# Kernel tuning notes

Hardware: AMD Instinct MI355X
Metric: run time of the kernel (lower is better)

Reference implementation:

```python
import jax, jax.numpy as jnp
import numpy as np


def setup_inputs() -> dict:
    key = jax.random.key(0)
    k1, k2, k3 = jax.random.split(key, 3)
    B, C, H, W = 16, 256, 48, 48
    INTER = C // 2
    x = jax.random.normal(k1, (B, C, H, W), dtype=jnp.float32)
    # nn.init.normal_(weight, std=0.01); 1x1 conv kernels stored as (out, in)
    theta_w = 0.01 * jax.random.normal(k2, (INTER, C), dtype=jnp.float32)
    phi_w = 0.01 * jax.random.normal(k3, (INTER, C), dtype=jnp.float32)
    theta_b = jnp.zeros((INTER,), dtype=jnp.float32)
    phi_b = jnp.zeros((INTER,), dtype=jnp.float32)
    return {"x": x, "theta_w": theta_w, "theta_b": theta_b, "phi_w": phi_w, "phi_b": phi_b}


def reference(x, theta_w, theta_b, phi_w, phi_b):
    b, c, h, w = x.shape
    inter = theta_w.shape[0]
    n = h * w
    # 1x1 conv == channel-wise linear projection
    theta_x = jnp.einsum('bchw,kc->bkhw', x, theta_w) + theta_b[None, :, None, None]
    phi_x = jnp.einsum('bchw,kc->bkhw', x, phi_w) + phi_b[None, :, None, None]
    q = theta_x.reshape(b, inter, n)   # [b, k, n]
    kmat = phi_x.reshape(b, inter, n)  # [b, k, n]
    g = x.reshape(b, c, n)             # [b, c, n]
    # f = theta^T @ phi : [b, n, n], scaled then softmaxed over last dim
    f = jnp.einsum('bkn,bkm->bnm', q, kmat) / jnp.sqrt(jnp.asarray(inter, x.dtype))
    f = jax.nn.softmax(f, axis=-1)
    # y = f @ g^T : [b, c, n]
    y = jnp.einsum('bnm,bcm->bcn', f, g)
    return y.reshape(b, c, h, w)
```

## Files before the change

### kernel.cpp

```cpp
#include <hip/hip_runtime.h>
#include <hip/hip_bf16.h>

#define B_SZ 16
#define C_IN 256
#define N_SP 2304
#define K_INT 128
#define NTILE 36
#define MT 32
#define MITER 72

typedef __attribute__((ext_vector_type(8))) short short8;
typedef __attribute__((ext_vector_type(4))) float f32x4;

__device__ __align__(16) short g_Wbf[2 * K_INT * C_IN];

__device__ inline unsigned pk_bf16(float a, float b) {
  float2 f; f.x = a; f.y = b;
  __hip_bfloat162 h = __float22bfloat162_rn(f);
  unsigned u;
  __builtin_memcpy(&u, &h, sizeof(u));
  return u;
}

__global__ __launch_bounds__(256) void wcvt_kernel(
    const float* __restrict__ tw, const float* __restrict__ pw)
{
  const int i = (blockIdx.x * 256 + threadIdx.x) * 4;
  float4 a = *(const float4*)(tw + i);
  float4 p = *(const float4*)(pw + i);
  uint2 ua; ua.x = pk_bf16(a.x, a.y); ua.y = pk_bf16(a.z, a.w);
  uint2 up; up.x = pk_bf16(p.x, p.y); up.y = pk_bf16(p.z, p.w);
  *(uint2*)(g_Wbf + i) = ua;
  *(uint2*)(g_Wbf + 32768 + i) = up;
}

__global__ __launch_bounds__(256) void proj_kernel(
    const float* __restrict__ x,
    const float* __restrict__ theta_b, const float* __restrict__ phi_b,
    short* __restrict__ Qt, short* __restrict__ Kt, short* __restrict__ Gbf)
{
  __shared__ short Xl[64][264];

  const int b  = blockIdx.x / NTILE;
  const int n0 = (blockIdx.x % NTILE) * 64;
  const int t  = threadIdx.x;

  {
    const int cr = t >> 4;
    const int a  = t & 15;
    const int n  = a * 4;
    const int g8 = (a & 3) << 3;
    const float* xs = x + ((size_t)b * C_IN + cr) * N_SP + n0 + n;
    short* gs = Gbf + ((size_t)b * C_IN + cr) * N_SP + n0 + n;
#pragma unroll
    for (int i = 0; i < 16; ++i) {
      float4 v = *(const float4*)(xs + (size_t)i * 16 * N_SP);
      unsigned p0 = pk_bf16(v.x, v.y), p1 = pk_bf16(v.z, v.w);
      uint2 u; u.x = p0; u.y = p1;
      *(uint2*)(gs + (size_t)i * 16 * N_SP) = u;
      const int cs0 = (cr + 16 * i) ^ g8;
      Xl[n + 0][cs0] = (short)p0;
      Xl[n + 1][cs0] = (short)(p0 >> 16);
      Xl[n + 2][cs0] = (short)p1;
      Xl[n + 3][cs0] = (short)(p1 >> 16);
    }
  }
  __syncthreads();

  const int wave = t >> 6, lane = t & 63;
  const int col = lane & 15, quad = lane >> 4;
  const int rg8 = ((col >> 2) & 3) << 3;

  f32x4 acc[2][2][4];
#pragma unroll
  for (int p = 0; p < 2; ++p)
#pragma unroll
    for (int kr = 0; kr < 2; ++kr)
#pragma unroll
      for (int j = 0; j < 4; ++j) {
        acc[p][kr][j][0] = 0.f; acc[p][kr][j][1] = 0.f;
        acc[p][kr][j][2] = 0.f; acc[p][kr][j][3] = 0.f;
      }

#pragma unroll
  for (int cs = 0; cs < 8; ++cs) {
    const int c0 = cs * 32;
    short8 afr[2][2];
#pragma unroll
    for (int p = 0; p < 2; ++p)
#pragma unroll
      for (int kr = 0; kr < 2; ++kr) {
        const int k = wave * 32 + kr * 16 + col;
        afr[p][kr] = *(const short8*)(g_Wbf + p * 32768 + k * C_IN + c0 + quad * 8);
      }
#pragma unroll
    for (int j = 0; j < 4; ++j) {
      short8 bfr = *(const short8*)&Xl[j * 16 + col][(c0 + quad * 8) ^ rg8];
#pragma unroll
      for (int p = 0; p < 2; ++p)
#pragma unroll
        for (int kr = 0; kr < 2; ++kr)
          acc[p][kr][j] = __builtin_amdgcn_mfma_f32_16x16x32_bf16(
              afr[p][kr], bfr, acc[p][kr][j], 0, 0, 0);
    }
  }

#pragma unroll
  for (int p = 0; p < 2; ++p) {
    const float* bias = p ? phi_b : theta_b;
    short* dst = p ? Kt : Qt;
#pragma unroll
    for (int kr = 0; kr < 2; ++kr) {
      const int k0 = wave * 32 + kr * 16 + quad * 4;
      float4 bv = *(const float4*)(bias + k0);
#pragma unroll
      for (int j = 0; j < 4; ++j) {
        const int n = n0 + j * 16 + col;
        f32x4 v = acc[p][kr][j];
        uint2 sv;
        sv.x = pk_bf16(v[0] + bv.x, v[1] + bv.y);
        sv.y = pk_bf16(v[2] + bv.z, v[3] + bv.w);
        *(uint2*)(dst + ((size_t)b * N_SP + n) * K_INT + k0) = sv;
      }
    }
  }
}

__global__ __launch_bounds__(256) void attn_kernel(
    const short* __restrict__ Qt, const short* __restrict__ Kt,
    const short* __restrict__ Gbf, float* __restrict__ out)
{
  __shared__ __align__(16) char Kl[2][8192];
  __shared__ __align__(16) short Pblob[2][4][64][8];
  __shared__ float l_lds[64];

  const int wg  = (blockIdx.x & 7) * 72 + (blockIdx.x >> 3);
  const int b   = wg / NTILE;
  const int qn0 = (wg % NTILE) * 64;
  const int t = threadIdx.x;
  const int wave = t >> 6, lane = t & 63;
  const int col = lane & 15, quad = lane >> 4;

  const short* Ktb = Kt  + (size_t)b * N_SP * K_INT;
  const short* Gb  = Gbf + (size_t)b * C_IN * N_SP;

  short8 qf[4];
  {
    const short* qb = Qt + ((size_t)b * N_SP + qn0 + wave * 16 + col) * K_INT + quad * 8;
#pragma unroll
    for (int kk = 0; kk < 4; ++kk) qf[kk] = *(const short8*)(qb + kk * 32);
  }

  f32x4 yacc[4][4];
#pragma unroll
  for (int i = 0; i < 4; ++i)
#pragma unroll
    for (int j = 0; j < 4; ++j) {
      yacc[i][j][0] = 0.f; yacc[i][j][1] = 0.f;
      yacc[i][j][2] = 0.f; yacc[i][j][3] = 0.f;
    }
  f32x4 lacc;
  lacc[0] = 0.f; lacc[1] = 0.f; lacc[2] = 0.f; lacc[3] = 0.f;

  short8 ones;
#pragma unroll
  for (int j = 0; j < 8; ++j) ones[j] = (short)0x3F80;

  const float SC2 = 0.12754859f;

  const int KW = (t >> 4) * 256 + ((((t & 15) ^ ((t >> 4) & 7))) << 4);
  int KR0[4];
#pragma unroll
  for (int kk = 0; kk < 4; ++kk)
    KR0[kk] = col * 256 + ((((kk << 2) + quad) ^ (col & 7)) << 4);

  const int koff = (t >> 4) * K_INT + (t & 15) * 8;
  const short* gbase = Gb + ((size_t)(wave * 64 + col)) * N_SP + quad * 8;

  short8 krA, krB;
  krA = *(const short8*)(Ktb + koff);
  krB = *(const short8*)(Ktb + 2048 + koff);
  *(short8*)(Kl[0] + KW) = krA;
  *(short8*)(Kl[0] + KW + 4096) = krB;
  krA = *(const short8*)(Ktb + 4096 + koff);
  krB = *(const short8*)(Ktb + 6144 + koff);
  short8 gA[4], gB[4];
#pragma unroll
  for (int ct = 0; ct < 4; ++ct)
    gA[ct] = *(const short8*)(gbase + (size_t)ct * 16 * N_SP);
  __syncthreads();

#define SUBITER(MTV, CUR, GC, GN)                                              \
  {                                                                            \
                           \
    f32x4 s0, s1;                                                              \
    s0[0] = 0.f; s0[1] = 0.f; s0[2] = 0.f; s0[3] = 0.f;                        \
    s1[0] = 0.f; s1[1] = 0.f; s1[2] = 0.f; s1[3] = 0.f;                        \
    _Pragma("unroll")                                                          \
    for (int kk = 0; kk < 4; ++kk) {                                           \
      short8 a0 = *(const short8*)(Kl[CUR] + KR0[kk]);                         \
      s0 = __builtin_amdgcn_mfma_f32_16x16x32_bf16(a0, qf[kk], s0, 0, 0, 0);   \
      short8 a1 = *(const short8*)(Kl[CUR] + KR0[kk] + 4096);                  \
      s1 = __builtin_amdgcn_mfma_f32_16x16x32_bf16(a1, qf[kk], s1, 0, 0, 0);   \
    }                                                                          \
                    \
    unsigned u0 = pk_bf16(exp2f(s0[0] * SC2), exp2f(s0[1] * SC2));             \
    unsigned u1 = pk_bf16(exp2f(s0[2] * SC2), exp2f(s0[3] * SC2));             \
    unsigned u2 = pk_bf16(exp2f(s1[0] * SC2), exp2f(s1[1] * SC2));             \
    unsigned u3 = pk_bf16(exp2f(s1[2] * SC2), exp2f(s1[3] * SC2));             \
    asm("v_permlane32_swap_b32 %0, %1" : "+v"(u0), "+v"(u2));                  \
    asm("v_permlane32_swap_b32 %0, %1" : "+v"(u1), "+v"(u3));                  \
    asm("v_permlane16_swap_b32 %0, %1" : "+v"(u0), "+v"(u2));                  \
    asm("v_permlane16_swap_b32 %0, %1" : "+v"(u1), "+v"(u3));                  \
    unsigned uu[4] = {u0, u1, u2, u3};                                         \
    short8 pa; __builtin_memcpy(&pa, uu, 16);                                  \
    lacc = __builtin_amdgcn_mfma_f32_16x16x32_bf16(pa, ones, lacc, 0, 0, 0);   \
                         \
    *(short8*)&Pblob[CUR][wave][lane][0] = pa;                                 \
        \
    if ((MTV) + 1 < MITER) {                                                   \
      *(short8*)(Kl[(CUR) ^ 1] + KW) = krA;                                    \
      *(short8*)(Kl[(CUR) ^ 1] + KW + 4096) = krB;                             \
    }                                                                          \
    __syncthreads();                                                           \
        \
    if ((MTV) + 2 < MITER) {                                                   \
      const short* kp = Ktb + (size_t)((MTV) + 2) * 4096 + koff;               \
      krA = *(const short8*)(kp);                                              \
      krB = *(const short8*)(kp + 2048);                                       \
    }                                                                          \
          \
    if ((MTV) + 1 < MITER) {                                                   \
      _Pragma("unroll")                                                        \
      for (int ct = 0; ct < 4; ++ct)                                           \
        GN[ct] = *(const short8*)(gbase + (size_t)ct * 16 * N_SP +             \
                                  ((MTV) + 1) * 32);                           \
    }                                                                          \
             \
    _Pragma("unroll")                                                          \
    for (int qt = 0; qt < 4; ++qt) {                                           \
      short8 paq = *(const short8*)&Pblob[CUR][qt][lane][0];                   \
      _Pragma("unroll")                                                        \
      for (int ct = 0; ct < 4; ++ct)                                           \
        yacc[qt][ct] = __builtin_amdgcn_mfma_f32_16x16x32_bf16(                \
            paq, GC[ct], yacc[qt][ct], 0, 0, 0);                               \
    }                                                                          \
  }

  for (int mt2 = 0; mt2 < MITER / 2; ++mt2) {
    SUBITER(2 * mt2,     0, gA, gB)
    SUBITER(2 * mt2 + 1, 1, gB, gA)
  }
#undef SUBITER

  if (col == 0) {
#pragma unroll
    for (int r = 0; r < 4; ++r) l_lds[wave * 16 + quad * 4 + r] = lacc[r];
  }
  __syncthreads();

#pragma unroll
  for (int qt = 0; qt < 4; ++qt) {
    float4 lq = *(const float4*)&l_lds[qt * 16 + quad * 4];
    float4 iv;
    iv.x = 1.0f / lq.x; iv.y = 1.0f / lq.y; iv.z = 1.0f / lq.z; iv.w = 1.0f / lq.w;
    const int nb = qn0 + qt * 16 + quad * 4;
#pragma unroll
    for (int ct = 0; ct < 4; ++ct) {
      const int c = wave * 64 + ct * 16 + col;
      f32x4 v = yacc[qt][ct];
      float4 o;
      o.x = v[0] * iv.x; o.y = v[1] * iv.y; o.z = v[2] * iv.z; o.w = v[3] * iv.w;
      *(float4*)(out + ((size_t)b * C_IN + c) * N_SP + nb) = o;
    }
  }
}

extern "C" void kernel_launch(void* const* d_in, const int* in_sizes, int n_in,
                              void* d_out, int out_size, void* d_ws, size_t ws_size,
                              hipStream_t stream) {
  const float* x  = (const float*)d_in[0];
  const float* tw = (const float*)d_in[1];
  const float* tb = (const float*)d_in[2];
  const float* pw = (const float*)d_in[3];
  const float* pb = (const float*)d_in[4];
  float* out = (float*)d_out;

  short* Qt  = (short*)d_ws;
  short* Kt  = Qt + (size_t)B_SZ * N_SP * K_INT;
  short* Gbf = Kt + (size_t)B_SZ * N_SP * K_INT;

  wcvt_kernel<<<32, 256, 0, stream>>>(tw, pw);
  proj_kernel<<<B_SZ * NTILE, 256, 0, stream>>>(x, tb, pb, Qt, Kt, Gbf);
  attn_kernel<<<B_SZ * NTILE, 256, 0, stream>>>(Qt, Kt, Gbf, out);
}
```

Measured before the change: 263.7 us.

## Double key tile per pipeline step to halve barriers in attention loop

Doubles the key-tile width processed per iteration from 32 to 64 positions, so each step computes four score MFMAs per k-slice, two P fragments, and sixteen extra PV MFMAs. It halves the number of __syncthreads barriers and prefetch rounds over the key dimension, and moves the global prefetches for K and G before the barrier. It also drops the block-index swizzle across XCDs. In exchange it uses more registers (8 G fragments, 4 K prefetch regs) and twice the LDS, which may lower occupancy, and the removed swizzle may hurt L2 locality.

```diff
diff --git a/kernel.cpp b/kernel.cpp
--- a/kernel.cpp
+++ b/kernel.cpp
@@ -6,8 +6,8 @@
 #define N_SP 2304
 #define K_INT 128
 #define NTILE 36
-#define MT 32
-#define MITER 72
+#define MT 64
+#define EITER 36
 
 typedef __attribute__((ext_vector_type(8))) short short8;
 typedef __attribute__((ext_vector_type(4))) float f32x4;
@@ -130,13 +130,12 @@
     const short* __restrict__ Qt, const short* __restrict__ Kt,
     const short* __restrict__ Gbf, float* __restrict__ out)
 {
-  __shared__ __align__(16) char Kl[2][8192];
-  __shared__ __align__(16) short Pblob[2][4][64][8];
+  __shared__ __align__(16) char Kl[2][16384];
+  __shared__ __align__(16) short Pblob[2][4][2][64][8];
   __shared__ float l_lds[64];
 
-  const int wg  = (blockIdx.x & 7) * 72 + (blockIdx.x >> 3);
-  const int b   = wg / NTILE;
-  const int qn0 = (wg % NTILE) * 64;
+  const int b   = blockIdx.x / NTILE;
+  const int qn0 = (blockIdx.x % NTILE) * 64;
   const int t = threadIdx.x;
   const int wave = t >> 6, lane = t & 63;
   const int col = lane & 15, quad = lane >> 4;
@@ -174,84 +173,108 @@
   for (int kk = 0; kk < 4; ++kk)
     KR0[kk] = col * 256 + ((((kk << 2) + quad) ^ (col & 7)) << 4);
 
-  const int koff = (t >> 4) * K_INT + (t & 15) * 8;
+  const int KG = (t >> 4) * K_INT + (t & 15) * 8;
   const short* gbase = Gb + ((size_t)(wave * 64 + col)) * N_SP + quad * 8;
 
-  short8 krA, krB;
-  krA = *(const short8*)(Ktb + koff);
-  krB = *(const short8*)(Ktb + 2048 + koff);
-  *(short8*)(Kl[0] + KW) = krA;
-  *(short8*)(Kl[0] + KW + 4096) = krB;
-  krA = *(const short8*)(Ktb + 4096 + koff);
-  krB = *(const short8*)(Ktb + 6144 + koff);
-  short8 gA[4], gB[4];
-#pragma unroll
-  for (int ct = 0; ct < 4; ++ct)
-    gA[ct] = *(const short8*)(gbase + (size_t)ct * 16 * N_SP);
+  short8 kr[4];
+#pragma unroll
+  for (int i = 0; i < 4; ++i) kr[i] = *(const short8*)(Ktb + KG + i * 2048);
+#pragma unroll
+  for (int i = 0; i < 4; ++i) *(short8*)(Kl[0] + KW + i * 4096) = kr[i];
+#pragma unroll
+  for (int i = 0; i < 4; ++i) kr[i] = *(const short8*)(Ktb + 8192 + KG + i * 2048);
+  short8 gA[8], gB[8];
+#pragma unroll
+  for (int i = 0; i < 8; ++i)
+    gA[i] = *(const short8*)(gbase + (size_t)(i & 3) * 16 * N_SP + (i >> 2) * 32);
   __syncthreads();
 
-#define SUBITER(MTV, CUR, GC, GN)                                              \
+#define EPOCH(EV, CUR, GC, GN)                                                 \
   {                                                                            \
-                           \
-    f32x4 s0, s1;                                                              \
-    s0[0] = 0.f; s0[1] = 0.f; s0[2] = 0.f; s0[3] = 0.f;                        \
-    s1[0] = 0.f; s1[1] = 0.f; s1[2] = 0.f; s1[3] = 0.f;                        \
+                         \
+    f32x4 s[4];                                                                \
+    _Pragma("unroll")                                                          \
+    for (int h = 0; h < 4; ++h) {                                              \
+      s[h][0] = 0.f; s[h][1] = 0.f; s[h][2] = 0.f; s[h][3] = 0.f;              \
+    }                                                                          \
     _Pragma("unroll")                                                          \
     for (int kk = 0; kk < 4; ++kk) {                                           \
-      short8 a0 = *(const short8*)(Kl[CUR] + KR0[kk]);                         \
-      s0 = __builtin_amdgcn_mfma_f32_16x16x32_bf16(a0, qf[kk], s0, 0, 0, 0);   \
-      short8 a1 = *(const short8*)(Kl[CUR] + KR0[kk] + 4096);                  \
-      s1 = __builtin_amdgcn_mfma_f32_16x16x32_bf16(a1, qf[kk], s1, 0, 0, 0);   \
-    }                                                                          \
-                    \
-    unsigned u0 = pk_bf16(exp2f(s0[0] * SC2), exp2f(s0[1] * SC2));             \
-    unsigned u1 = pk_bf16(exp2f(s0[2] * SC2), exp2f(s0[3] * SC2));             \
-    unsigned u2 = pk_bf16(exp2f(s1[0] * SC2), exp2f(s1[1] * SC2));             \
-    unsigned u3 = pk_bf16(exp2f(s1[2] * SC2), exp2f(s1[3] * SC2));             \
-    asm("v_permlane32_swap_b32 %0, %1" : "+v"(u0), "+v"(u2));                  \
-    asm("v_permlane32_swap_b32 %0, %1" : "+v"(u1), "+v"(u3));                  \
-    asm("v_permlane16_swap_b32 %0, %1" : "+v"(u0), "+v"(u2));                  \
-    asm("v_permlane16_swap_b32 %0, %1" : "+v"(u1), "+v"(u3));                  \
-    unsigned uu[4] = {u0, u1, u2, u3};                                         \
-    short8 pa; __builtin_memcpy(&pa, uu, 16);                                  \
-    lacc = __builtin_amdgcn_mfma_f32_16x16x32_bf16(pa, ones, lacc, 0, 0, 0);   \
-                         \
-    *(short8*)&Pblob[CUR][wave][lane][0] = pa;                                 \
-        \
-    if ((MTV) + 1 < MITER) {                                                   \
-      *(short8*)(Kl[(CUR) ^ 1] + KW) = krA;                                    \
-      *(short8*)(Kl[(CUR) ^ 1] + KW + 4096) = krB;                             \
+      _Pragma("unroll")                                                        \
+      for (int h = 0; h < 4; ++h) {                                            \
+        short8 a0 = *(const short8*)(Kl[CUR] + KR0[kk] + h * 4096);            \
+        s[h] = __builtin_amdgcn_mfma_f32_16x16x32_bf16(a0, qf[kk], s[h],       \
+                                                       0, 0, 0);               \
+      }                                                                        \
+    }                                                                          \
+                 \
+    short8 pa0, pa1;                                                           \
+    {                                                                          \
+      unsigned u0 = pk_bf16(exp2f(s[0][0] * SC2), exp2f(s[0][1] * SC2));       \
+      unsigned u1 = pk_bf16(exp2f(s[0][2] * SC2), exp2f(s[0][3] * SC2));       \
+      unsigned u2 = pk_bf16(exp2f(s[1][0] * SC2), exp2f(s[1][1] * SC2));       \
+      unsigned u3 = pk_bf16(exp2f(s[1][2] * SC2), exp2f(s[1][3] * SC2));       \
+      asm("v_permlane32_swap_b32 %0, %1" : "+v"(u0), "+v"(u2));                \
+      asm("v_permlane32_swap_b32 %0, %1" : "+v"(u1), "+v"(u3));                \
+      asm("v_permlane16_swap_b32 %0, %1" : "+v"(u0), "+v"(u2));                \
+      asm("v_permlane16_swap_b32 %0, %1" : "+v"(u1), "+v"(u3));                \
+      unsigned uu[4] = {u0, u1, u2, u3};                                       \
+      __builtin_memcpy(&pa0, uu, 16);                                          \
+      unsigned v0 = pk_bf16(exp2f(s[2][0] * SC2), exp2f(s[2][1] * SC2));       \
+      unsigned v1 = pk_bf16(exp2f(s[2][2] * SC2), exp2f(s[2][3] * SC2));       \
+      unsigned v2 = pk_bf16(exp2f(s[3][0] * SC2), exp2f(s[3][1] * SC2));       \
+      unsigned v3 = pk_bf16(exp2f(s[3][2] * SC2), exp2f(s[3][3] * SC2));       \
+      asm("v_permlane32_swap_b32 %0, %1" : "+v"(v0), "+v"(v2));                \
+      asm("v_permlane32_swap_b32 %0, %1" : "+v"(v1), "+v"(v3));                \
+      asm("v_permlane16_swap_b32 %0, %1" : "+v"(v0), "+v"(v2));                \
+      asm("v_permlane16_swap_b32 %0, %1" : "+v"(v1), "+v"(v3));                \
+      unsigned vv[4] = {v0, v1, v2, v3};                                       \
+      __builtin_memcpy(&pa1, vv, 16);                                          \
+    }                                                                          \
+    lacc = __builtin_amdgcn_mfma_f32_16x16x32_bf16(pa0, ones, lacc, 0, 0, 0);  \
+    lacc = __builtin_amdgcn_mfma_f32_16x16x32_bf16(pa1, ones, lacc, 0, 0, 0);  \
+                        \
+    *(short8*)&Pblob[CUR][wave][0][lane][0] = pa0;                             \
+    *(short8*)&Pblob[CUR][wave][1][lane][0] = pa1;                             \
+       \
+    if ((EV) + 1 < EITER) {                                                    \
+      _Pragma("unroll")                                                        \
+      for (int i = 0; i < 4; ++i)                                              \
+        *(short8*)(Kl[(CUR) ^ 1] + KW + i * 4096) = kr[i];                     \
+    }                                                                          \
+                     \
+    if ((EV) + 2 < EITER) {                                                    \
+      const short* kp = Ktb + (size_t)((EV) + 2) * 8192 + KG;                  \
+      _Pragma("unroll")                                                        \
+      for (int i = 0; i < 4; ++i) kr[i] = *(const short8*)(kp + i * 2048);     \
+    }                                                                          \
+              \
+    if ((EV) + 1 < EITER) {                                                    \
+      _Pragma("unroll")                                                        \
+      for (int i = 0; i < 8; ++i)                                              \
+        GN[i] = *(const short8*)(gbase + (size_t)(i & 3) * 16 * N_SP +         \
+                                 ((EV) + 1) * 64 + (i >> 2) * 32);             \
     }                                                                          \
     __syncthreads();                                                           \
-        \
-    if ((MTV) + 2 < MITER) {                                                   \
-      const short* kp = Ktb + (size_t)((MTV) + 2) * 4096 + koff;               \
-      krA = *(const short8*)(kp);                                              \
-      krB = *(const short8*)(kp + 2048);                                       \
-    }                                                                          \
-          \
-    if ((MTV) + 1 < MITER) {                                                   \
-      _Pragma("unroll")                                                        \
-      for (int ct = 0; ct < 4; ++ct)                                           \
-        GN[ct] = *(const short8*)(gbase + (size_t)ct * 16 * N_SP +             \
-                                  ((MTV) + 1) * 32);                           \
-    }                                                                          \
-             \
+              \
     _Pragma("unroll")                                                          \
     for (int qt = 0; qt < 4; ++qt) {                                           \
-      short8 paq = *(const short8*)&Pblob[CUR][qt][lane][0];                   \
-      _Pragma("unroll")                                                        \
-      for (int ct = 0; ct < 4; ++ct)                                           \
+      short8 paq0 = *(const short8*)&Pblob[CUR][qt][0][lane][0];               \
+      short8 paq1 = *(const short8*)&Pblob[CUR][qt][1][lane][0];               \
+      _Pragma("unroll")                                                        \
+      for (int ct = 0; ct < 4; ++ct) {                                         \
         yacc[qt][ct] = __builtin_amdgcn_mfma_f32_16x16x32_bf16(                \
-            paq, GC[ct], yacc[qt][ct], 0, 0, 0);                               \
-    }                                                                          \
-  }
-
-  for (int mt2 = 0; mt2 < MITER / 2; ++mt2) {
-    SUBITER(2 * mt2,     0, gA, gB)
-    SUBITER(2 * mt2 + 1, 1, gB, gA)
-  }
-#undef SUBITER
+            paq0, GC[ct], yacc[qt][ct], 0, 0, 0);                              \
+        yacc[qt][ct] = __builtin_amdgcn_mfma_f32_16x16x32_bf16(                \
+            paq1, GC[4 + ct], yacc[qt][ct], 0, 0, 0);                          \
+      }                                                                        \
+    }                                                                          \
+  }
+
+  for (int e2 = 0; e2 < EITER / 2; ++e2) {
+    EPOCH(2 * e2,     0, gA, gB)
+    EPOCH(2 * e2 + 1, 1, gB, gA)
+  }
+#undef EPOCH
 
   if (col == 0) {
 #pragma unroll
```

Measured after the change: 289.9 us. 9.9% more time.
